# Performance work log

Hardware: AMD Instinct MI355X
Metric: run time of the kernel (lower is better)

## Reference

```python
import jax, jax.numpy as jnp
import numpy as np

NUM_GROUPS = 256


def _linear(x, w, b):
    return x @ w + b


def _layernorm(x, g, b, eps=1e-5):
    mu = jnp.mean(x, axis=-1, keepdims=True)
    var = jnp.mean((x - mu) ** 2, axis=-1, keepdims=True)
    return (x - mu) / jnp.sqrt(var + eps) * g + b


def setup_inputs() -> dict:
    key = jax.random.key(0)
    ks = jax.random.split(key, 12)
    B, N, C = 16, 8192, 3
    s = 0.02
    return {
        "xyz": jax.random.normal(ks[0], (B, N, C), jnp.float32),
        "labels": jax.random.randint(ks[1], (B, N), 0, NUM_GROUPS),
        # conv1: Linear(3,128) -> LayerNorm(128) -> ReLU -> Linear(128,256)
        "w1a": jax.random.normal(ks[2], (3, 128), jnp.float32) * s,
        "b1a": jnp.zeros((128,), jnp.float32),
        "g1": jnp.ones((128,), jnp.float32),
        "beta1": jnp.zeros((128,), jnp.float32),
        "w1b": jax.random.normal(ks[3], (128, 256), jnp.float32) * s,
        "b1b": jnp.zeros((256,), jnp.float32),
        # conv2: Linear(512,512) -> LayerNorm(512) -> ReLU -> Linear(512,256)
        "w2a": jax.random.normal(ks[4], (512, 512), jnp.float32) * s,
        "b2a": jnp.zeros((512,), jnp.float32),
        "g2": jnp.ones((512,), jnp.float32),
        "beta2": jnp.zeros((512,), jnp.float32),
        "w2b": jax.random.normal(ks[5], (512, 256), jnp.float32) * s,
        "b2b": jnp.zeros((256,), jnp.float32),
    }


def reference(xyz, labels, w1a, b1a, g1, beta1, w1b, b1b,
              w2a, b2a, g2, beta2, w2b, b2b):
    # per-batch segment reductions over cluster labels
    seg_sum = jax.vmap(lambda f, l: jax.ops.segment_sum(f, l, num_segments=NUM_GROUPS))
    seg_max = jax.vmap(lambda f, l: jax.ops.segment_max(f, l, num_segments=NUM_GROUPS))
    gather = jax.vmap(lambda p, l: p[l])  # [G,D],[N] -> [N,D]

    # centroids = per-cluster mean of xyz (converged kmeans centroids)
    counts = seg_sum(jnp.ones_like(xyz[..., :1]), labels)          # [B,G,1]
    centroids = seg_sum(xyz, labels) / jnp.maximum(counts, 1.0)    # [B,G,3]

    p_i = gather(centroids, labels)                                # [B,N,3]
    relative_xyz = xyz - p_i                                       # feature_type='dp'

    h = _linear(relative_xyz, w1a, b1a)
    h = jax.nn.relu(_layernorm(h, g1, beta1))
    h = _linear(h, w1b, b1b)                                       # [B,N,256]

    pooled = seg_max(h, labels)                                    # [B,G,256]
    pooled = jnp.where(jnp.isfinite(pooled), pooled, 0.0)          # empty groups -> 0
    repeated = gather(pooled, labels)                              # [B,N,256]

    cat = jnp.concatenate([repeated, h], axis=-1)                  # [B,N,512]
    h2 = _linear(cat, w2a, b2a)
    h2 = jax.nn.relu(_layernorm(h2, g2, beta2))
    h2 = _linear(h2, w2b, b2b)                                     # [B,N,256]

    out = seg_max(h2, labels)                                      # [B,G,256]
    out = jnp.where(jnp.isfinite(out), out, 0.0)
    return (centroids, out, p_i, labels)
```

## Files before the change

### kernel.cpp

```cpp
#include <hip/hip_runtime.h>
#include <hip/hip_bf16.h>

#define NB_  16
#define NPTS 8192
#define NG   256
#define NP   (NB_*NPTS)
#define NBLK (NP/64)

#define OFF_CENT 0
#define OFF_OUT  12288
#define OFF_PI   1060864
#define OFF_LAB  1454080

typedef unsigned short u16;
typedef __attribute__((ext_vector_type(8))) short bf16x8;
typedef __attribute__((ext_vector_type(4))) float f32x4;

static constexpr size_t WS_SUMS  = 0;
static constexpr size_t WS_A1    = 65536;
static constexpr size_t WS_H     = WS_A1   + (size_t)NP*128*2;
static constexpr size_t WS_PBF   = WS_H    + (size_t)NP*256*2;
static constexpr size_t WS_WT1   = WS_PBF  + (size_t)NB_*NG*256*2;
static constexpr size_t WS_WT2A  = WS_WT1  + (size_t)256*128*2;
static constexpr size_t WS_WT2B  = WS_WT2A + (size_t)512*512*2;
static constexpr size_t WS_PREP  = WS_WT2B + (size_t)256*512*2;
static constexpr size_t WS_OFFS  = WS_PREP + (size_t)NB_*NG*512*4;
static constexpr size_t WS_CNT   = WS_OFFS + (size_t)NB_*NG*4;
static constexpr size_t WS_CUR   = WS_CNT  + (size_t)NB_*NG*4;
static constexpr size_t WS_SPOS  = WS_CUR  + (size_t)NB_*NG*4;
static constexpr size_t WS_GLAB  = WS_SPOS + (size_t)NP*4;
static constexpr size_t WS_PF    = WS_GLAB + (size_t)NP*4;
static constexpr size_t WS_PL    = WS_PF   + (size_t)NBLK*256*4;
static constexpr size_t WS_DST   = WS_PL   + (size_t)NBLK*256*4;
static constexpr size_t WS_NEED  = WS_DST  + (size_t)NB_*NG*256*4;

__device__ __forceinline__ u16 f2bf_bits(float f){
  __hip_bfloat16 h = __float2bfloat16(f);
  union { __hip_bfloat16 h; u16 s; } u; u.h = h; return u.s;
}
__device__ __forceinline__ float bf_bits2f(u16 s){
  return __uint_as_float(((unsigned)s) << 16);
}

__device__ __forceinline__ void gload16(const void* g, void* l){
  __builtin_amdgcn_global_load_lds((const __attribute__((address_space(1))) void*)g,
                                   (__attribute__((address_space(3))) void*)l, 16, 0, 0);
}

__global__ void k_init(float* __restrict__ sums, int* __restrict__ cursor){
  int i = blockIdx.x*blockDim.x + threadIdx.x;
  if (i < NB_*NG*4) sums[i] = 0.f;
  if (i < NB_*NG) cursor[i] = 0;
}

__global__ void k_wt(const float* __restrict__ src, u16* __restrict__ dst, int K, int N){
  int i = blockIdx.x*blockDim.x + threadIdx.x;
  if (i >= K*N) return;
  int n = i / K, k = i - n*K;
  dst[i] = f2bf_bits(src[(size_t)k*N + n]);
}

__global__ void k_points(const float* __restrict__ xyz, const int* __restrict__ labels,
                         float* __restrict__ sums, float* __restrict__ outLab){
  int p = blockIdx.x*blockDim.x + threadIdx.x;
  if (p >= NP) return;
  int b = p / NPTS;
  int g = labels[p];
  float x = xyz[p*3+0], y = xyz[p*3+1], z = xyz[p*3+2];
  float* s = sums + (size_t)(b*NG + g)*4;
  atomicAdd(s+0, x); atomicAdd(s+1, y); atomicAdd(s+2, z); atomicAdd(s+3, 1.f);
  outLab[p] = (float)g;
}

__global__ void k_cent(const float* __restrict__ sums, float* __restrict__ cent_out){
  int i = blockIdx.x*blockDim.x + threadIdx.x;
  if (i >= NB_*NG) return;
  const float* s = sums + (size_t)i*4;
  float c = fmaxf(s[3], 1.f);
  cent_out[i*3+0] = s[0]/c;
  cent_out[i*3+1] = s[1]/c;
  cent_out[i*3+2] = s[2]/c;
}

__global__ void k_scan(const float* __restrict__ sums, int* __restrict__ offs,
                       int* __restrict__ counts){
  __shared__ int sc[256];
  int b = blockIdx.x, g = threadIdx.x;
  int c = (int)(sums[(size_t)(b*NG+g)*4+3] + 0.5f);
  sc[g] = c;
  __syncthreads();
  for (int d = 1; d < 256; d <<= 1){
    int t = (g >= d) ? sc[g-d] : 0;
    __syncthreads();
    sc[g] += t;
    __syncthreads();
  }
  offs[b*NG+g] = b*NPTS + sc[g] - c;
  counts[b*NG+g] = c;
}

__global__ void k_scatter(const int* __restrict__ labels, const int* __restrict__ offs,
                          int* __restrict__ cursor, int* __restrict__ sortpos,
                          int* __restrict__ glab){
  int p = blockIdx.x*blockDim.x + threadIdx.x;
  if (p >= NP) return;
  int b = p / NPTS, g = labels[p];
  int pos = offs[b*NG+g] + atomicAdd(&cursor[b*NG+g], 1);
  sortpos[p] = pos;
  glab[pos] = g;
}

__global__ __launch_bounds__(256) void k_mlp1(
    const float* __restrict__ xyz, const int* __restrict__ labels,
    const int* __restrict__ sortpos, const float* __restrict__ cent,
    const float* __restrict__ w1a, const float* __restrict__ b1a,
    const float* __restrict__ g1, const float* __restrict__ beta1,
    u16* __restrict__ a1, float* __restrict__ pi_out)
{
  int wave = (int)((blockIdx.x*blockDim.x + threadIdx.x) >> 6);
  int lane = threadIdx.x & 63;
  int p = wave;
  if (p >= NP) return;
  int b = p / NPTS;
  int g = labels[p];
  const float* cb = cent + (size_t)(b*NG+g)*3;
  float c0 = cb[0], c1 = cb[1], c2 = cb[2];
  float r0 = xyz[p*3+0]-c0, r1 = xyz[p*3+1]-c1, r2 = xyz[p*3+2]-c2;
  if (lane < 3) pi_out[(size_t)p*3+lane] = (lane==0?c0:(lane==1?c1:c2));
  int j = lane*2;
  float2 wa0 = *(const float2*)(w1a + 0*128 + j);
  float2 wa1 = *(const float2*)(w1a + 1*128 + j);
  float2 wa2 = *(const float2*)(w1a + 2*128 + j);
  float2 bb  = *(const float2*)(b1a + j);
  float t0 = bb.x + r0*wa0.x + r1*wa1.x + r2*wa2.x;
  float t1 = bb.y + r0*wa0.y + r1*wa1.y + r2*wa2.y;
  float s = t0+t1, sq = t0*t0 + t1*t1;
  #pragma unroll
  for (int m = 32; m; m >>= 1){ s += __shfl_xor(s, m); sq += __shfl_xor(sq, m); }
  float mu  = s * (1.f/128.f);
  float var = sq * (1.f/128.f) - mu*mu;
  float inv = rsqrtf(var + 1e-5f);
  float2 gg = *(const float2*)(g1 + j), be = *(const float2*)(beta1 + j);
  float a0 = fmaxf((t0-mu)*inv*gg.x + be.x, 0.f);
  float a1v = fmaxf((t1-mu)*inv*gg.y + be.y, 0.f);
  unsigned pk = ((unsigned)f2bf_bits(a1v) << 16) | f2bf_bits(a0);
  int sp = sortpos[p];
  *reinterpret_cast<unsigned*>(a1 + (size_t)sp*128 + j) = pk;
}

template<int EPI>
__global__ __launch_bounds__(256)
void mgemm(const u16* __restrict__ A, int lda, int K,
           const u16* __restrict__ BT, int ldb, int kofs,
           const float* __restrict__ bias,
           u16* __restrict__ Cst, float* __restrict__ Cf, int ldc, int Nc)
{
  __shared__ alignas(16) u16 As[128*32];
  __shared__ alignas(16) u16 Bs[128*32];
  int NBk = Nc >> 7;
  int bm = blockIdx.x / NBk, bn = blockIdx.x % NBk;
  int m0 = bm << 7, n0 = bn << 7;
  int tid = threadIdx.x;
  int lane = tid & 63, w = tid >> 6;
  int wr = w >> 1, wc = w & 1;
  int l15 = lane & 15, l4 = lane >> 4;
  int r0 = tid >> 2;
  int ks = (tid & 3) << 3;
  u16* asd0 = As + (size_t)(w*64)*8;
  u16* asd1 = As + (size_t)(256 + w*64)*8;
  u16* bsd0 = Bs + (size_t)(w*64)*8;
  u16* bsd1 = Bs + (size_t)(256 + w*64)*8;
  f32x4 acc[4][4];
  #pragma unroll
  for (int i = 0; i < 4; ++i)
    #pragma unroll
    for (int jj = 0; jj < 4; ++jj)
      #pragma unroll
      for (int e = 0; e < 4; ++e) acc[i][jj][e] = 0.f;

  for (int k0 = 0; k0 < K; k0 += 32){
    gload16(A + (size_t)(m0 + r0)*lda + k0 + ks, asd0);
    gload16(A + (size_t)(m0 + r0 + 64)*lda + k0 + ks, asd1);
    gload16(BT + (size_t)(n0 + r0)*ldb + kofs + k0 + ks, bsd0);
    gload16(BT + (size_t)(n0 + r0 + 64)*ldb + kofs + k0 + ks, bsd1);
    __syncthreads();
    bf16x8 af[4], bfr[4];
    #pragma unroll
    for (int i = 0; i < 4; ++i){
      af[i]  = *(const bf16x8*)&As[(size_t)(wr*64 + i*16 + l15)*32 + l4*8];
      bfr[i] = *(const bf16x8*)&Bs[(size_t)(wc*64 + i*16 + l15)*32 + l4*8];
    }
    #pragma unroll
    for (int i = 0; i < 4; ++i)
      #pragma unroll
      for (int jj = 0; jj < 4; ++jj)
        acc[i][jj] = __builtin_amdgcn_mfma_f32_16x16x32_bf16(af[i], bfr[jj], acc[i][jj], 0, 0, 0);
    __syncthreads();
  }

  float bi[4];
  #pragma unroll
  for (int jj = 0; jj < 4; ++jj) bi[jj] = bias[n0 + wc*64 + jj*16 + l15];
  #pragma unroll
  for (int i = 0; i < 4; ++i){
    #pragma unroll
    for (int r = 0; r < 4; ++r){
      int m = m0 + wr*64 + i*16 + l4*4 + r;
      #pragma unroll
      for (int jj = 0; jj < 4; ++jj){
        int n = n0 + wc*64 + jj*16 + l15;
        float v = acc[i][jj][r] + bi[jj];
        if (EPI == 1) Cst[(size_t)m*ldc + n] = f2bf_bits(v);
        if (EPI == 3) Cf[(size_t)m*ldc + n] = v;
      }
    }
  }
}

__global__ __launch_bounds__(256) void k_pool(const u16* __restrict__ h,
                                              const int* __restrict__ offs,
                                              const int* __restrict__ counts,
                                              u16* __restrict__ poolbf){
  int bg = blockIdx.x, c = threadIdx.x;
  int cnt = counts[bg];
  if (cnt == 0){ poolbf[(size_t)bg*256 + c] = 0; return; }
  int off = offs[bg];
  float mx = bf_bits2f(h[(size_t)off*256 + c]);
  for (int r = 1; r < cnt; ++r)
    mx = fmaxf(mx, bf_bits2f(h[(size_t)(off+r)*256 + c]));
  poolbf[(size_t)bg*256 + c] = f2bf_bits(mx);
}

__global__ __launch_bounds__(512, 2)
void fused4(const u16* __restrict__ h, const u16* __restrict__ wt2a,
            const u16* __restrict__ wt2b, const float* __restrict__ prepf,
            const float* __restrict__ b2b, const float* __restrict__ g2,
            const float* __restrict__ beta2, const int* __restrict__ glab,
            float* __restrict__ pf, float* __restrict__ pl, float* __restrict__ dstage)
{
  __shared__ alignas(16) char smem[66560];
  float* ssum  = (float*)(smem + 65536);
  float* ssq   = (float*)(smem + 65792);
  int*  glab_s = (int*)(smem + 66048);
  int tid = threadIdx.x;
  int w = tid >> 6, lane = tid & 63;
  int l15 = lane & 15, l4 = lane >> 4;
  int m0 = blockIdx.x << 6;
  if (tid < 64){ ssum[tid] = 0.f; ssq[tid] = 0.f; glab_s[tid] = glab[m0 + tid]; }

  {
    const char* hb = (const char*)h;
    int lrow = lane >> 5;
    int kb = (lane & 31) << 4;
    #pragma unroll
    for (int t = 0; t < 4; ++t){
      int q = w*4 + t;
      int row = q*2 + lrow;
      gload16(hb + (size_t)(m0 + row)*512 + (kb ^ ((row & 7) << 4)),
              smem + q*1024);
    }
  }
  f32x4 acc[4][4];
  #pragma unroll
  for (int i = 0; i < 4; ++i)
    #pragma unroll
    for (int j = 0; j < 4; ++j)
      #pragma unroll
      for (int e = 0; e < 4; ++e) acc[i][j][e] = 0.f;
  __syncthreads();

  for (int k0 = 0; k0 < 256; k0 += 32){
    bf16x8 af[4], bfr[4];
    #pragma unroll
    for (int i = 0; i < 4; ++i){
      int row = (i<<4) + l15;
      af[i] = *(const bf16x8*)(smem + row*512 + ((((k0 + l4*8)) << 1) ^ ((row & 7) << 4)));
    }
    #pragma unroll
    for (int j = 0; j < 4; ++j){
      int n = (w<<6) + (j<<4) + l15;
      bfr[j] = *(const bf16x8*)(wt2a + (size_t)n*512 + 256 + k0 + l4*8);
    }
    #pragma unroll
    for (int i = 0; i < 4; ++i)
      #pragma unroll
      for (int j = 0; j < 4; ++j)
        acc[i][j] = __builtin_amdgcn_mfma_f32_16x16x32_bf16(af[i], bfr[j], acc[i][j], 0, 0, 0);
  }

  int gb = (m0 / NPTS) * NG;
  {
    int grp[4][4];
    #pragma unroll
    for (int i = 0; i < 4; ++i)
      #pragma unroll
      for (int r = 0; r < 4; ++r)
        grp[i][r] = gb + glab_s[(i<<4) + (l4<<2) + r];
    #pragma unroll
    for (int i = 0; i < 4; ++i)
      #pragma unroll
      for (int j = 0; j < 4; ++j){
        int n = (w<<6) + (j<<4) + l15;
        #pragma unroll
        for (int r = 0; r < 4; ++r)
          acc[i][j][r] += prepf[((size_t)grp[i][r] << 9) + n];
      }
  }
  #pragma unroll
  for (int i = 0; i < 4; ++i)
    #pragma unroll
    for (int r = 0; r < 4; ++r){
      float s = 0.f, q = 0.f;
      #pragma unroll
      for (int j = 0; j < 4; ++j){ float v = acc[i][j][r]; s += v; q += v*v; }
      #pragma unroll
      for (int mk = 1; mk < 16; mk <<= 1){ s += __shfl_xor(s, mk); q += __shfl_xor(q, mk); }
      if (l15 == 0){
        int row = (i<<4) + (l4<<2) + r;
        atomicAdd(&ssum[row], s);
        atomicAdd(&ssq[row], q);
      }
    }
  __syncthreads();
  if (tid < 64){
    float mu = ssum[tid] * (1.f/512.f);
    float var = ssq[tid] * (1.f/512.f) - mu*mu;
    ssum[tid] = mu;
    ssq[tid] = rsqrtf(var + 1e-5f);
  }
  __syncthreads();
  {
    float gcol[4], bcol[4];
    #pragma unroll
    for (int j = 0; j < 4; ++j){
      int n = (w<<6) + (j<<4) + l15;
      gcol[j] = g2[n]; bcol[j] = beta2[n];
    }
    #pragma unroll
    for (int i = 0; i < 4; ++i)
      #pragma unroll
      for (int r = 0; r < 4; ++r){
        int row = (i<<4) + (l4<<2) + r;
        float mu = ssum[row], inv = ssq[row];
        #pragma unroll
        for (int j = 0; j < 4; ++j){
          int n = (w<<6) + (j<<4) + l15;
          float v = fmaxf((acc[i][j][r] - mu)*inv*gcol[j] + bcol[j], 0.f);
          int byo = (row << 10) + (((n << 1)) ^ ((row & 7) << 4));
          *(u16*)(smem + byo) = f2bf_bits(v);
        }
      }
  }
  __syncthreads();

  f32x4 acc2[4][2];
  #pragma unroll
  for (int i = 0; i < 4; ++i)
    #pragma unroll
    for (int j = 0; j < 2; ++j)
      #pragma unroll
      for (int e = 0; e < 4; ++e) acc2[i][j][e] = 0.f;

  for (int k0 = 0; k0 < 512; k0 += 32){
    bf16x8 af2[4], bf2[2];
    #pragma unroll
    for (int i = 0; i < 4; ++i){
      int row = (i<<4) + l15;
      af2[i] = *(const bf16x8*)(smem + (row << 10) + ((((k0 + l4*8)) << 1) ^ ((row & 7) << 4)));
    }
    #pragma unroll
    for (int j = 0; j < 2; ++j){
      int n = (w<<5) + (j<<4) + l15;
      bf2[j] = *(const bf16x8*)(wt2b + (size_t)n*512 + k0 + l4*8);
    }
    #pragma unroll
    for (int i = 0; i < 4; ++i)
      #pragma unroll
      for (int j = 0; j < 2; ++j)
        acc2[i][j] = __builtin_amdgcn_mfma_f32_16x16x32_bf16(af2[i], bf2[j], acc2[i][j], 0, 0, 0);
  }
  __syncthreads();

  float bb0 = b2b[(w<<5) + l15], bb1 = b2b[(w<<5) + 16 + l15];
  float* vbuf = (float*)smem;
  #pragma unroll
  for (int i = 0; i < 4; ++i)
    #pragma unroll
    for (int j = 0; j < 2; ++j){
      int n = (w<<5) + (j<<4) + l15;
      float bbj = j ? bb1 : bb0;
      #pragma unroll
      for (int r = 0; r < 4; ++r){
        int row = (i<<4) + (l4<<2) + r;
        vbuf[row*256 + n] = acc2[i][j][r] + bbj;
      }
    }
  __syncthreads();
  if (tid < 256){
    int c = tid;
    size_t blk = blockIdx.x;
    int curg = glab_s[0];
    float mx = vbuf[c];
    bool from0 = true;
    for (int r = 1; r < 64; ++r){
      int g = glab_s[r];
      float v = vbuf[r*256 + c];
      if (g != curg){
        if (from0) pf[blk*256 + c] = mx;
        else       dstage[((size_t)(gb + curg))*256 + c] = mx;
        curg = g; mx = v; from0 = false;
      } else mx = fmaxf(mx, v);
    }
    if (from0) pf[blk*256 + c] = mx;
    else       pl[blk*256 + c] = mx;
  }
}

__global__ __launch_bounds__(256) void k_combine(const int* __restrict__ offs,
                                                 const int* __restrict__ counts,
                                                 const float* __restrict__ pf,
                                                 const float* __restrict__ pl,
                                                 const float* __restrict__ dstage,
                                                 float* __restrict__ outp){
  int bg = blockIdx.x, c = threadIdx.x;
  int cnt = counts[bg];
  if (cnt == 0){ outp[(size_t)bg*256 + c] = 0.f; return; }
  int off = offs[bg], end = off + cnt;
  int B0 = off >> 6, B1 = (end - 1) >> 6;
  float v;
  if (B0 == B1){
    if ((off & 63) == 0)      v = pf[(size_t)B0*256 + c];
    else if ((end & 63) == 0) v = pl[(size_t)B0*256 + c];
    else                      v = dstage[(size_t)bg*256 + c];
  } else {
    v = ((off & 63) == 0) ? pf[(size_t)B0*256 + c] : pl[(size_t)B0*256 + c];
    for (int k = B0 + 1; k <= B1; ++k)
      v = fmaxf(v, pf[(size_t)k*256 + c]);
  }
  outp[(size_t)bg*256 + c] = v;
}

__global__ void k_sig(float* __restrict__ out, float val){
  int i = blockIdx.x*blockDim.x + threadIdx.x;
  if (i < 256) out[i] = val;
}

extern "C" void kernel_launch(void* const* d_in, const int* in_sizes, int n_in,
                              void* d_out, int out_size, void* d_ws, size_t ws_size,
                              hipStream_t stream) {
  const float* xyz    = (const float*)d_in[0];
  const int*   labels = (const int*)  d_in[1];
  const float* w1a    = (const float*)d_in[2];
  const float* b1a    = (const float*)d_in[3];
  const float* g1     = (const float*)d_in[4];
  const float* beta1  = (const float*)d_in[5];
  const float* w1b    = (const float*)d_in[6];
  const float* b1b    = (const float*)d_in[7];
  const float* w2a    = (const float*)d_in[8];
  const float* b2a    = (const float*)d_in[9];
  const float* g2     = (const float*)d_in[10];
  const float* beta2  = (const float*)d_in[11];
  const float* w2b    = (const float*)d_in[12];
  const float* b2b    = (const float*)d_in[13];
  float* out = (float*)d_out;
  char* ws = (char*)d_ws;

  if (ws_size < WS_NEED){
    k_sig<<<1, 256, 0, stream>>>(out, 10000.f + (float)(ws_size >> 20));
    return;
  }

  float*     sums   = (float*)(ws + WS_SUMS);
  u16*       a1     = (u16*)(ws + WS_A1);
  u16*       h      = (u16*)(ws + WS_H);
  u16*       poolbf = (u16*)(ws + WS_PBF);
  u16*       wt1    = (u16*)(ws + WS_WT1);
  u16*       wt2a   = (u16*)(ws + WS_WT2A);
  u16*       wt2b   = (u16*)(ws + WS_WT2B);
  float*     prepf  = (float*)(ws + WS_PREP);
  int*       offs   = (int*)(ws + WS_OFFS);
  int*       counts = (int*)(ws + WS_CNT);
  int*       cursor = (int*)(ws + WS_CUR);
  int*       sortpos= (int*)(ws + WS_SPOS);
  int*       glab   = (int*)(ws + WS_GLAB);
  float*     pf     = (float*)(ws + WS_PF);
  float*     pl     = (float*)(ws + WS_PL);
  float*     dstage = (float*)(ws + WS_DST);

  float* cent_out = out + OFF_CENT;
  float* out_seg  = out + OFF_OUT;
  float* pi_out   = out + OFF_PI;
  float* lab_out  = out + OFF_LAB;

  k_init<<<64, 256, 0, stream>>>(sums, cursor);
  k_wt<<<(128*256+255)/256, 256, 0, stream>>>(w1b, wt1, 128, 256);
  k_wt<<<(512*512+255)/256, 256, 0, stream>>>(w2a, wt2a, 512, 512);
  k_wt<<<(512*256+255)/256, 256, 0, stream>>>(w2b, wt2b, 512, 256);
  k_points<<<NP/256, 256, 0, stream>>>(xyz, labels, sums, lab_out);
  k_cent<<<(NB_*NG+255)/256, 256, 0, stream>>>(sums, cent_out);
  k_scan<<<NB_, 256, 0, stream>>>(sums, offs, counts);
  k_scatter<<<NP/256, 256, 0, stream>>>(labels, offs, cursor, sortpos, glab);
  k_mlp1<<<NP/4, 256, 0, stream>>>(xyz, labels, sortpos, cent_out,
                                   w1a, b1a, g1, beta1, a1, pi_out);
  mgemm<1><<<(NP/128)*(256/128), 256, 0, stream>>>(
      a1, 128, 128, wt1, 128, 0, b1b, h, (float*)nullptr, 256, 256);
  k_pool<<<NB_*NG, 256, 0, stream>>>(h, offs, counts, poolbf);
  mgemm<3><<<(NB_*NG/128)*(512/128), 256, 0, stream>>>(
      poolbf, 256, 256, wt2a, 512, 0, b2a, (u16*)nullptr, prepf, 512, 512);
  fused4<<<NBLK, 512, 0, stream>>>(h, wt2a, wt2b, prepf, b2b, g2, beta2, glab,
                                   pf, pl, dstage);
  k_combine<<<NB_*NG, 256, 0, stream>>>(offs, counts, pf, pl, dstage, out_seg);
}
```

Baseline: 370.4 us.

## Double fused MLP row tile to 128 with 1024-thread blocks for weight reuse

The fused second-MLP kernel now processes 128 points per block instead of 64, using 16 waves and about 130 KB of LDS. Each wave covers all 8 row tiles with narrower column slices, so each weight fragment loaded from global memory feeds twice as many MFMAs. This roughly halves total weight traffic across the grid. The k_combine block-boundary logic is updated to the 128-row granularity to match. In exchange, only one block fits per CU, and the serial per-column segment-max epilogue walks twice as many rows. The grid is also halved, which may worsen tail balance.

```diff
diff --git a/kernel.cpp b/kernel.cpp
--- a/kernel.cpp
+++ b/kernel.cpp
@@ -5,7 +5,7 @@
 #define NPTS 8192
 #define NG   256
 #define NP   (NB_*NPTS)
-#define NBLK (NP/64)
+#define NBLK (NP/128)
 
 #define OFF_CENT 0
 #define OFF_OUT  12288
@@ -231,22 +231,22 @@
   poolbf[(size_t)bg*256 + c] = f2bf_bits(mx);
 }
 
-__global__ __launch_bounds__(512, 2)
-void fused4(const u16* __restrict__ h, const u16* __restrict__ wt2a,
+__global__ __launch_bounds__(1024, 1)
+void fused6(const u16* __restrict__ h, const u16* __restrict__ wt2a,
             const u16* __restrict__ wt2b, const float* __restrict__ prepf,
             const float* __restrict__ b2b, const float* __restrict__ g2,
             const float* __restrict__ beta2, const int* __restrict__ glab,
             float* __restrict__ pf, float* __restrict__ pl, float* __restrict__ dstage)
 {
-  __shared__ alignas(16) char smem[66560];
-  float* ssum  = (float*)(smem + 65536);
-  float* ssq   = (float*)(smem + 65792);
-  int*  glab_s = (int*)(smem + 66048);
+  __shared__ alignas(16) char smem[132608];
+  float* ssum  = (float*)(smem + 131072);
+  float* ssq   = (float*)(smem + 131584);
+  int*  glab_s = (int*)(smem + 132096);
   int tid = threadIdx.x;
   int w = tid >> 6, lane = tid & 63;
   int l15 = lane & 15, l4 = lane >> 4;
-  int m0 = blockIdx.x << 6;
-  if (tid < 64){ ssum[tid] = 0.f; ssq[tid] = 0.f; glab_s[tid] = glab[m0 + tid]; }
+  int m0 = blockIdx.x << 7;
+  if (tid < 128){ ssum[tid] = 0.f; ssq[tid] = 0.f; glab_s[tid] = glab[m0 + tid]; }
 
   {
     const char* hb = (const char*)h;
@@ -260,59 +260,58 @@
               smem + q*1024);
     }
   }
-  f32x4 acc[4][4];
-  #pragma unroll
-  for (int i = 0; i < 4; ++i)
-    #pragma unroll
-    for (int j = 0; j < 4; ++j)
+  f32x4 acc[8][2];
+  #pragma unroll
+  for (int i = 0; i < 8; ++i)
+    #pragma unroll
+    for (int j = 0; j < 2; ++j)
       #pragma unroll
       for (int e = 0; e < 4; ++e) acc[i][j][e] = 0.f;
   __syncthreads();
 
-  for (int k0 = 0; k0 < 256; k0 += 32){
-    bf16x8 af[4], bfr[4];
-    #pragma unroll
-    for (int i = 0; i < 4; ++i){
-      int row = (i<<4) + l15;
-      af[i] = *(const bf16x8*)(smem + row*512 + ((((k0 + l4*8)) << 1) ^ ((row & 7) << 4)));
-    }
-    #pragma unroll
-    for (int j = 0; j < 4; ++j){
-      int n = (w<<6) + (j<<4) + l15;
-      bfr[j] = *(const bf16x8*)(wt2a + (size_t)n*512 + 256 + k0 + l4*8);
-    }
-    #pragma unroll
-    for (int i = 0; i < 4; ++i)
-      #pragma unroll
-      for (int j = 0; j < 4; ++j)
-        acc[i][j] = __builtin_amdgcn_mfma_f32_16x16x32_bf16(af[i], bfr[j], acc[i][j], 0, 0, 0);
+  {
+    const u16* wA = wt2a + ((size_t)((w<<5) + l15))*512 + 256 + l4*8;
+    #pragma unroll
+    for (int kk = 0; kk < 8; ++kk){
+      const int k0 = kk*32;
+      bf16x8 af[8], bfr[2];
+      #pragma unroll
+      for (int j = 0; j < 2; ++j)
+        bfr[j] = *(const bf16x8*)(wA + j*8192 + k0);
+      #pragma unroll
+      for (int i = 0; i < 8; ++i){
+        int row = (i<<4) + l15;
+        af[i] = *(const bf16x8*)(smem + row*512 + ((((k0 + l4*8)) << 1) ^ ((row & 7) << 4)));
+      }
+      #pragma unroll
+      for (int i = 0; i < 8; ++i)
+        #pragma unroll
+        for (int j = 0; j < 2; ++j)
+          acc[i][j] = __builtin_amdgcn_mfma_f32_16x16x32_bf16(af[i], bfr[j], acc[i][j], 0, 0, 0);
+    }
   }
 
   int gb = (m0 / NPTS) * NG;
-  {
-    int grp[4][4];
-    #pragma unroll
-    for (int i = 0; i < 4; ++i)
-      #pragma unroll
-      for (int r = 0; r < 4; ++r)
-        grp[i][r] = gb + glab_s[(i<<4) + (l4<<2) + r];
-    #pragma unroll
-    for (int i = 0; i < 4; ++i)
-      #pragma unroll
-      for (int j = 0; j < 4; ++j){
-        int n = (w<<6) + (j<<4) + l15;
-        #pragma unroll
-        for (int r = 0; r < 4; ++r)
-          acc[i][j][r] += prepf[((size_t)grp[i][r] << 9) + n];
+  #pragma unroll
+  for (int i = 0; i < 8; ++i){
+    #pragma unroll
+    for (int r = 0; r < 4; ++r){
+      int row = (i<<4) + (l4<<2) + r;
+      int grp = gb + glab_s[row];
+      #pragma unroll
+      for (int j = 0; j < 2; ++j){
+        int n = (w<<5) + (j<<4) + l15;
+        acc[i][j][r] += prepf[((size_t)grp << 9) + n];
       }
-  }
-  #pragma unroll
-  for (int i = 0; i < 4; ++i)
+    }
+  }
+  #pragma unroll
+  for (int i = 0; i < 8; ++i)
     #pragma unroll
     for (int r = 0; r < 4; ++r){
       float s = 0.f, q = 0.f;
       #pragma unroll
-      for (int j = 0; j < 4; ++j){ float v = acc[i][j][r]; s += v; q += v*v; }
+      for (int j = 0; j < 2; ++j){ float v = acc[i][j][r]; s += v; q += v*v; }
       #pragma unroll
       for (int mk = 1; mk < 16; mk <<= 1){ s += __shfl_xor(s, mk); q += __shfl_xor(q, mk); }
       if (l15 == 0){
@@ -322,7 +321,7 @@
       }
     }
   __syncthreads();
-  if (tid < 64){
+  if (tid < 128){
     float mu = ssum[tid] * (1.f/512.f);
     float var = ssq[tid] * (1.f/512.f) - mu*mu;
     ssum[tid] = mu;
@@ -330,21 +329,21 @@
   }
   __syncthreads();
   {
-    float gcol[4], bcol[4];
-    #pragma unroll
-    for (int j = 0; j < 4; ++j){
-      int n = (w<<6) + (j<<4) + l15;
+    float gcol[2], bcol[2];
+    #pragma unroll
+    for (int j = 0; j < 2; ++j){
+      int n = (w<<5) + (j<<4) + l15;
       gcol[j] = g2[n]; bcol[j] = beta2[n];
     }
     #pragma unroll
-    for (int i = 0; i < 4; ++i)
+    for (int i = 0; i < 8; ++i)
       #pragma unroll
       for (int r = 0; r < 4; ++r){
         int row = (i<<4) + (l4<<2) + r;
         float mu = ssum[row], inv = ssq[row];
         #pragma unroll
-        for (int j = 0; j < 4; ++j){
-          int n = (w<<6) + (j<<4) + l15;
+        for (int j = 0; j < 2; ++j){
+          int n = (w<<5) + (j<<4) + l15;
           float v = fmaxf((acc[i][j][r] - mu)*inv*gcol[j] + bcol[j], 0.f);
           int byo = (row << 10) + (((n << 1)) ^ ((row & 7) << 4));
           *(u16*)(smem + byo) = f2bf_bits(v);
@@ -353,48 +352,42 @@
   }
   __syncthreads();
 
-  f32x4 acc2[4][2];
-  #pragma unroll
-  for (int i = 0; i < 4; ++i)
-    #pragma unroll
-    for (int j = 0; j < 2; ++j)
-      #pragma unroll
-      for (int e = 0; e < 4; ++e) acc2[i][j][e] = 0.f;
-
-  for (int k0 = 0; k0 < 512; k0 += 32){
-    bf16x8 af2[4], bf2[2];
-    #pragma unroll
-    for (int i = 0; i < 4; ++i){
-      int row = (i<<4) + l15;
-      af2[i] = *(const bf16x8*)(smem + (row << 10) + ((((k0 + l4*8)) << 1) ^ ((row & 7) << 4)));
-    }
-    #pragma unroll
-    for (int j = 0; j < 2; ++j){
-      int n = (w<<5) + (j<<4) + l15;
-      bf2[j] = *(const bf16x8*)(wt2b + (size_t)n*512 + k0 + l4*8);
-    }
-    #pragma unroll
-    for (int i = 0; i < 4; ++i)
-      #pragma unroll
-      for (int j = 0; j < 2; ++j)
-        acc2[i][j] = __builtin_amdgcn_mfma_f32_16x16x32_bf16(af2[i], bf2[j], acc2[i][j], 0, 0, 0);
-  }
-  __syncthreads();
-
-  float bb0 = b2b[(w<<5) + l15], bb1 = b2b[(w<<5) + 16 + l15];
+  f32x4 acc2[8];
+  #pragma unroll
+  for (int i = 0; i < 8; ++i)
+    #pragma unroll
+    for (int e = 0; e < 4; ++e) acc2[i][e] = 0.f;
+
+  {
+    const u16* wB = wt2b + ((size_t)((w<<4) + l15))*512 + l4*8;
+    #pragma unroll
+    for (int kk = 0; kk < 16; ++kk){
+      const int k0 = kk*32;
+      bf16x8 af2[8], bf2;
+      bf2 = *(const bf16x8*)(wB + k0);
+      #pragma unroll
+      for (int i = 0; i < 8; ++i){
+        int row = (i<<4) + l15;
+        af2[i] = *(const bf16x8*)(smem + (row << 10) + ((((k0 + l4*8)) << 1) ^ ((row & 7) << 4)));
+      }
+      #pragma unroll
+      for (int i = 0; i < 8; ++i)
+        acc2[i] = __builtin_amdgcn_mfma_f32_16x16x32_bf16(af2[i], bf2, acc2[i], 0, 0, 0);
+    }
+  }
+  __syncthreads();
+
+  float bb = b2b[(w<<4) + l15];
   float* vbuf = (float*)smem;
   #pragma unroll
-  for (int i = 0; i < 4; ++i)
-    #pragma unroll
-    for (int j = 0; j < 2; ++j){
-      int n = (w<<5) + (j<<4) + l15;
-      float bbj = j ? bb1 : bb0;
-      #pragma unroll
-      for (int r = 0; r < 4; ++r){
-        int row = (i<<4) + (l4<<2) + r;
-        vbuf[row*256 + n] = acc2[i][j][r] + bbj;
-      }
-    }
+  for (int i = 0; i < 8; ++i){
+    int n = (w<<4) + l15;
+    #pragma unroll
+    for (int r = 0; r < 4; ++r){
+      int row = (i<<4) + (l4<<2) + r;
+      vbuf[row*256 + n] = acc2[i][r] + bb;
+    }
+  }
   __syncthreads();
   if (tid < 256){
     int c = tid;
@@ -402,7 +395,7 @@
     int curg = glab_s[0];
     float mx = vbuf[c];
     bool from0 = true;
-    for (int r = 1; r < 64; ++r){
+    for (int r = 1; r < 128; ++r){
       int g = glab_s[r];
       float v = vbuf[r*256 + c];
       if (g != curg){
@@ -426,14 +419,14 @@
   int cnt = counts[bg];
   if (cnt == 0){ outp[(size_t)bg*256 + c] = 0.f; return; }
   int off = offs[bg], end = off + cnt;
-  int B0 = off >> 6, B1 = (end - 1) >> 6;
+  int B0 = off >> 7, B1 = (end - 1) >> 7;
   float v;
   if (B0 == B1){
-    if ((off & 63) == 0)      v = pf[(size_t)B0*256 + c];
-    else if ((end & 63) == 0) v = pl[(size_t)B0*256 + c];
-    else                      v = dstage[(size_t)bg*256 + c];
+    if ((off & 127) == 0)      v = pf[(size_t)B0*256 + c];
+    else if ((end & 127) == 0) v = pl[(size_t)B0*256 + c];
+    else                       v = dstage[(size_t)bg*256 + c];
   } else {
-    v = ((off & 63) == 0) ? pf[(size_t)B0*256 + c] : pl[(size_t)B0*256 + c];
+    v = ((off & 127) == 0) ? pf[(size_t)B0*256 + c] : pl[(size_t)B0*256 + c];
     for (int k = B0 + 1; k <= B1; ++k)
       v = fmaxf(v, pf[(size_t)k*256 + c]);
   }
@@ -507,7 +500,7 @@
   k_pool<<<NB_*NG, 256, 0, stream>>>(h, offs, counts, poolbf);
   mgemm<3><<<(NB_*NG/128)*(512/128), 256, 0, stream>>>(
       poolbf, 256, 256, wt2a, 512, 0, b2a, (u16*)nullptr, prepf, 512, 512);
-  fused4<<<NBLK, 512, 0, stream>>>(h, wt2a, wt2b, prepf, b2b, g2, beta2, glab,
-                                   pf, pl, dstage);
+  fused6<<<NBLK, 1024, 0, stream>>>(h, wt2a, wt2b, prepf, b2b, g2, beta2, glab,
+                                    pf, pl, dstage);
   k_combine<<<NB_*NG, 256, 0, stream>>>(offs, counts, pf, pl, dstage, out_seg);
 }
```

New measurement: 371.2 us. No clear change (+0.2%).
